# Performance work log

Measured on AMD Instinct MI355X. Metric: run time of the kernel, lower is better.

## Reference

```python
import jax, jax.numpy as jnp
import numpy as np

D_MODEL = 512
D_STATE = 128
D_CONV = 4
EXPAND = 2
NL = 10
HEADDIM = 64
D_INNER = EXPAND * D_MODEL            # 1024
NHEADS = D_INNER // HEADDIM           # 16
CONV_DIM = D_INNER + 2 * D_STATE      # 1280
D_PROJ = 2 * D_INNER + 2 * D_STATE + NHEADS  # 2320
BATCH = 8
IN_S, TOK_S = 3647, 64                # -> 57 tokens
IN_G, TOK_G = 18, 2                   # -> 9 tokens
NCLS = 55
CA_HEADS = 8
EPS = 1e-5


def setup_inputs() -> dict:
    key = jax.random.key(0)
    ks = iter(jax.random.split(key, 80))
    nrm = lambda shape, s=0.02: jax.random.normal(next(ks), shape, jnp.float32) * s
    inp = {
        "x_spectra": jax.random.normal(next(ks), (BATCH, IN_S), jnp.float32),
        "x_gaia": jax.random.normal(next(ks), (BATCH, IN_G), jnp.float32),
        "tok_w_s": nrm((TOK_S, D_MODEL), 0.05), "tok_b_s": jnp.zeros((D_MODEL,)),
        "tok_w_g": nrm((TOK_G, D_MODEL), 0.05), "tok_b_g": jnp.zeros((D_MODEL,)),
    }
    for p in ("ms", "mg"):  # spectra / gaia Mamba2 stacks, params stacked over layers
        inp[p + "_Win"] = nrm((NL, D_MODEL, D_PROJ))
        inp[p + "_conv_w"] = nrm((NL, CONV_DIM, D_CONV), 0.1)
        inp[p + "_conv_b"] = jnp.zeros((NL, CONV_DIM))
        inp[p + "_dt_bias"] = nrm((NL, NHEADS), 0.5)
        inp[p + "_A_log"] = jnp.log(jnp.tile(jnp.arange(1, NHEADS + 1, dtype=jnp.float32), (NL, 1)))
        inp[p + "_D"] = jnp.ones((NL, NHEADS))
        inp[p + "_norm_w"] = jnp.ones((NL, D_INNER))
        inp[p + "_Wout"] = nrm((NL, D_INNER, D_MODEL))
    for p in ("ca_s", "ca_g"):  # cross-attention blocks
        inp[p + "_ln_w"] = jnp.ones((D_MODEL,)); inp[p + "_ln_b"] = jnp.zeros((D_MODEL,))
        inp[p + "_in_w"] = nrm((3 * D_MODEL, D_MODEL)); inp[p + "_in_b"] = jnp.zeros((3 * D_MODEL,))
        inp[p + "_out_w"] = nrm((D_MODEL, D_MODEL)); inp[p + "_out_b"] = jnp.zeros((D_MODEL,))
    inp["cls_ln_w"] = jnp.ones((2 * D_MODEL,)); inp["cls_ln_b"] = jnp.zeros((2 * D_MODEL,))
    inp["cls_w"] = nrm((NCLS, 2 * D_MODEL)); inp["cls_b"] = jnp.zeros((NCLS,))
    return inp


def _ln(x, w, b):
    m = x.mean(-1, keepdims=True)
    v = jnp.var(x, -1, keepdims=True)
    return (x - m) * jax.lax.rsqrt(v + EPS) * w + b


def _tokenize(x, in_dim, tok_dim, w, b):
    bsz = x.shape[0]
    ntok = -(-in_dim // tok_dim)
    x = jnp.pad(x, ((0, 0), (0, ntok * tok_dim - in_dim)))
    return x.reshape(bsz, ntok, tok_dim) @ w + b  # [B, ntok, d_model]


def _mamba2_layer(x, Win, conv_w, conv_b, dt_bias, A_log, Dp, norm_w, Wout):
    bsz, L, _ = x.shape
    zxbcdt = x @ Win  # [B,L,D_PROJ]
    z, xBC, dt = jnp.split(zxbcdt, [D_INNER, D_INNER + CONV_DIM], axis=-1)
    # causal depthwise conv over time (kernel D_CONV), then SiLU
    xp = jnp.pad(xBC, ((0, 0), (D_CONV - 1, 0), (0, 0)))
    xBC = sum(conv_w[:, k] * xp[:, k:k + L, :] for k in range(D_CONV)) + conv_b
    xBC = jax.nn.silu(xBC)
    xh, Bm, Cm = jnp.split(xBC, [D_INNER, D_INNER + D_STATE], axis=-1)
    dt = jax.nn.softplus(dt + dt_bias)                 # [B,L,H]
    A = -jnp.exp(A_log)                                # [H]
    xh = xh.reshape(bsz, L, NHEADS, HEADDIM)
    dA = jnp.exp(dt * A)                               # [B,L,H] in (0,1)
    dBx = jnp.einsum('blh,bln,blhp->blhpn', dt, Bm, xh)
    # h_t = dA_t * h_{t-1} + dBx_t  via parallel associative scan over time
    def comb(e1, e2):
        a1, b1 = e1
        a2, b2 = e2
        return a1 * a2, a2[..., None, None] * b1 + b2
    _, h = jax.lax.associative_scan(comb, (dA, dBx), axis=1)  # h: [B,L,H,P,N]
    y = jnp.einsum('blhpn,bln->blhp', h, Cm) + Dp[None, None, :, None] * xh
    y = y.reshape(bsz, L, D_INNER)
    # gated RMSNorm (norm_before_gate=False): rmsnorm(y * silu(z)) * w
    y = y * jax.nn.silu(z)
    y = y * jax.lax.rsqrt(jnp.mean(y * y, -1, keepdims=True) + EPS) * norm_w
    return y @ Wout


def _mamba_stack(x, Win, cw, cb, dtb, Alog, Dp, nw, Wout):
    for i in range(NL):
        x = _mamba2_layer(x, Win[i], cw[i], cb[i], dtb[i], Alog[i], Dp[i], nw[i], Wout[i])
    return x


def _mha(q, kv, in_w, in_b, out_w, out_b):
    E = D_MODEL
    hd = E // CA_HEADS
    wq, wk, wv = in_w[:E], in_w[E:2 * E], in_w[2 * E:]
    bq, bk, bv = in_b[:E], in_b[E:2 * E], in_b[2 * E:]
    qh = (q @ wq.T + bq).reshape(*q.shape[:2], CA_HEADS, hd)
    kh = (kv @ wk.T + bk).reshape(*kv.shape[:2], CA_HEADS, hd)
    vh = (kv @ wv.T + bv).reshape(*kv.shape[:2], CA_HEADS, hd)
    scores = jnp.einsum('bqhd,bkhd->bhqk', qh, kh) / np.sqrt(hd).astype(np.float32)
    attn = jax.nn.softmax(scores, axis=-1)
    out = jnp.einsum('bhqk,bkhd->bqhd', attn, vh).reshape(*q.shape[:2], E)
    return out @ out_w.T + out_b


def reference(x_spectra, x_gaia, tok_w_s, tok_b_s, tok_w_g, tok_b_g,
              ms_Win, ms_conv_w, ms_conv_b, ms_dt_bias, ms_A_log, ms_D, ms_norm_w, ms_Wout,
              mg_Win, mg_conv_w, mg_conv_b, mg_dt_bias, mg_A_log, mg_D, mg_norm_w, mg_Wout,
              ca_s_ln_w, ca_s_ln_b, ca_s_in_w, ca_s_in_b, ca_s_out_w, ca_s_out_b,
              ca_g_ln_w, ca_g_ln_b, ca_g_in_w, ca_g_in_b, ca_g_out_w, ca_g_out_b,
              cls_ln_w, cls_ln_b, cls_w, cls_b):
    xs = _tokenize(x_spectra, IN_S, TOK_S, tok_w_s, tok_b_s)   # [B,57,512]
    xg = _tokenize(x_gaia, IN_G, TOK_G, tok_w_g, tok_b_g)      # [B,9,512]
    xs = _mamba_stack(xs, ms_Win, ms_conv_w, ms_conv_b, ms_dt_bias, ms_A_log, ms_D, ms_norm_w, ms_Wout)
    xg = _mamba_stack(xg, mg_Win, mg_conv_w, mg_conv_b, mg_dt_bias, mg_A_log, mg_D, mg_norm_w, mg_Wout)
    # cross attention (note: gaia attends to the UPDATED spectra, as in the torch code)
    xs = xs + _mha(_ln(xs, ca_s_ln_w, ca_s_ln_b), xg, ca_s_in_w, ca_s_in_b, ca_s_out_w, ca_s_out_b)
    xg = xg + _mha(_ln(xg, ca_g_ln_w, ca_g_ln_b), xs, ca_g_in_w, ca_g_in_b, ca_g_out_w, ca_g_out_b)
    fused = jnp.concatenate([xs.mean(1), xg.mean(1)], axis=-1)  # [B,1024]
    return _ln(fused, cls_ln_w, cls_ln_b) @ cls_w.T + cls_b      # [B,55]
```

## Files before the change

kernel.cpp:

```cpp
#include <hip/hip_runtime.h>
#include <cmath>

constexpr int BB    = 8;
constexpr int LS    = 57;
constexpr int LG    = 9;
constexpr int RS    = BB*LS;
constexpr int RG    = BB*LG;
constexpr int DM    = 512;
constexpr int DPROJ = 2320;
constexpr int DIN   = 1024;
constexpr int NH    = 16;
constexpr int HD    = 64;
constexpr int NLAY  = 10;

constexpr int SP_IN  = 4;
constexpr int SP_OUT = 8;
constexpr int SP_ATT = 4;

__device__ __forceinline__ float siluf(float x){ return x / (1.f + expf(-x)); }

typedef short  short8 __attribute__((ext_vector_type(8)));
typedef float  f32x4  __attribute__((ext_vector_type(4)));

__device__ __forceinline__ unsigned short f2bh(float f){
    unsigned int u = __float_as_uint(f);
    u = u + 0x7FFFu + ((u >> 16) & 1u);
    return (unsigned short)(u >> 16);
}
__device__ __forceinline__ float bh2f(unsigned short h){
    return __uint_as_float(((unsigned int)h) << 16);
}

__global__ __launch_bounds__(512) void tokenize_k(
    const float* __restrict__ x, const float* __restrict__ w, const float* __restrict__ bias,
    float* __restrict__ out, int in_dim, int tok_dim, int ntok)
{
    int t = blockIdx.x, b = blockIdx.y, d = threadIdx.x;
    __shared__ float xv[64];
    if (d < tok_dim) {
        int idx = t*tok_dim + d;
        xv[d] = (idx < in_dim) ? x[(size_t)b*in_dim + idx] : 0.f;
    }
    __syncthreads();
    float acc = bias[d];
    for (int k=0;k<tok_dim;k++) acc += xv[k]*w[(size_t)k*DM + d];
    out[(size_t)(b*ntok + t)*DM + d] = acc;
}

struct GemmJob {
    const float* A; const float* B; float* part; int M;
};

template<bool TB, int NSPLIT>
__global__ __launch_bounds__(256) void gemm_mfma(GemmJob j0, GemmJob j1, GemmJob j2, int N, int K)
{
    const int z = blockIdx.z;
    const int job = z / NSPLIT, split = z % NSPLIT;
    GemmJob jb = (job==0) ? j0 : (job==1 ? j1 : j2);
    const int bm = blockIdx.y*64, bn = blockIdx.x*64;
    const int M = jb.M;
    if (bm >= M) return;

    constexpr int SR = 40;
    __shared__ unsigned short Ah[64*SR], Al[64*SR];
    __shared__ unsigned short Bh[64*SR], Bl[64*SR];

    const int tid = threadIdx.x;
    const float* __restrict__ A  = jb.A;
    const float* __restrict__ Bm = jb.B;

    const int ar = tid >> 2, ac0 = (tid & 3) * 8;
    const int wkN = tid >> 3, wcN0 = (tid & 7) * 8;
    const int wnT = tid >> 2, wkT0 = (tid & 3) * 8;

    float a_reg[8];
    float w_reg[8];

    auto loadA = [&](int k0){
        if (bm + ar < M){
            const float* src = A + (size_t)(bm+ar)*K + k0 + ac0;
            float4 v0 = *(const float4*)(src);
            float4 v1 = *(const float4*)(src+4);
            a_reg[0]=v0.x; a_reg[1]=v0.y; a_reg[2]=v0.z; a_reg[3]=v0.w;
            a_reg[4]=v1.x; a_reg[5]=v1.y; a_reg[6]=v1.z; a_reg[7]=v1.w;
        } else {
            #pragma unroll
            for (int j=0;j<8;j++) a_reg[j]=0.f;
        }
    };
    auto loadW = [&](int k0){
        if constexpr (!TB){
            const float* src = Bm + (size_t)(k0+wkN)*N + bn + wcN0;
            if (bn + wcN0 + 4 <= N){
                float4 v0 = *(const float4*)(src);
                float4 v1 = *(const float4*)(src+4);
                w_reg[0]=v0.x; w_reg[1]=v0.y; w_reg[2]=v0.z; w_reg[3]=v0.w;
                w_reg[4]=v1.x; w_reg[5]=v1.y; w_reg[6]=v1.z; w_reg[7]=v1.w;
            } else if (bn + wcN0 < N){
                float4 v0 = *(const float4*)(src);
                w_reg[0]=v0.x; w_reg[1]=v0.y; w_reg[2]=v0.z; w_reg[3]=v0.w;
                w_reg[4]=0.f; w_reg[5]=0.f; w_reg[6]=0.f; w_reg[7]=0.f;
            } else {
                #pragma unroll
                for (int j=0;j<8;j++) w_reg[j]=0.f;
            }
        } else {
            if (bn + wnT < N){
                const float* src = Bm + (size_t)(bn+wnT)*K + k0 + wkT0;
                float4 v0 = *(const float4*)(src);
                float4 v1 = *(const float4*)(src+4);
                w_reg[0]=v0.x; w_reg[1]=v0.y; w_reg[2]=v0.z; w_reg[3]=v0.w;
                w_reg[4]=v1.x; w_reg[5]=v1.y; w_reg[6]=v1.z; w_reg[7]=v1.w;
            } else {
                #pragma unroll
                for (int j=0;j<8;j++) w_reg[j]=0.f;
            }
        }
    };
    auto storeT = [&](){
        #pragma unroll
        for (int j=0;j<8;j++){
            const unsigned short h = f2bh(a_reg[j]);
            const unsigned short lo = f2bh(a_reg[j] - bh2f(h));
            Ah[ar*SR + ac0 + j] = h;
            Al[ar*SR + ac0 + j] = lo;
        }
        if constexpr (!TB){
            #pragma unroll
            for (int j=0;j<8;j++){
                const unsigned short h = f2bh(w_reg[j]);
                const unsigned short lo = f2bh(w_reg[j] - bh2f(h));
                Bh[(wcN0+j)*SR + wkN] = h;
                Bl[(wcN0+j)*SR + wkN] = lo;
            }
        } else {
            #pragma unroll
            for (int j=0;j<8;j++){
                const unsigned short h = f2bh(w_reg[j]);
                const unsigned short lo = f2bh(w_reg[j] - bh2f(h));
                Bh[wnT*SR + wkT0 + j] = h;
                Bl[wnT*SR + wkT0 + j] = lo;
            }
        }
    };

    const int Kper = K / NSPLIT;
    const int koff = split * Kper;
    const int nk   = Kper / 32;

    const int l  = tid & 63, w = tid >> 6;
    const int fr = l & 15, kg = (l >> 4) * 8;

    f32x4 acc0 = {0.f,0.f,0.f,0.f};
    f32x4 acc1 = {0.f,0.f,0.f,0.f};
    f32x4 acc2 = {0.f,0.f,0.f,0.f};
    f32x4 acc3 = {0.f,0.f,0.f,0.f};

    loadA(koff); loadW(koff);
    for (int t=0; t<nk; ++t){
        storeT();
        __syncthreads();
        if (t+1 < nk){ loadA(koff+(t+1)*32); loadW(koff+(t+1)*32); }

        const short8 ah = *(const short8*)&Ah[(w*16+fr)*SR + kg];
        const short8 al = *(const short8*)&Al[(w*16+fr)*SR + kg];
        {
            const short8 bh = *(const short8*)&Bh[(fr)*SR + kg];
            const short8 bl = *(const short8*)&Bl[(fr)*SR + kg];
            acc0 = __builtin_amdgcn_mfma_f32_16x16x32_bf16(ah, bh, acc0, 0,0,0);
            acc0 = __builtin_amdgcn_mfma_f32_16x16x32_bf16(ah, bl, acc0, 0,0,0);
            acc0 = __builtin_amdgcn_mfma_f32_16x16x32_bf16(al, bh, acc0, 0,0,0);
        }
        {
            const short8 bh = *(const short8*)&Bh[(16+fr)*SR + kg];
            const short8 bl = *(const short8*)&Bl[(16+fr)*SR + kg];
            acc1 = __builtin_amdgcn_mfma_f32_16x16x32_bf16(ah, bh, acc1, 0,0,0);
            acc1 = __builtin_amdgcn_mfma_f32_16x16x32_bf16(ah, bl, acc1, 0,0,0);
            acc1 = __builtin_amdgcn_mfma_f32_16x16x32_bf16(al, bh, acc1, 0,0,0);
        }
        {
            const short8 bh = *(const short8*)&Bh[(32+fr)*SR + kg];
            const short8 bl = *(const short8*)&Bl[(32+fr)*SR + kg];
            acc2 = __builtin_amdgcn_mfma_f32_16x16x32_bf16(ah, bh, acc2, 0,0,0);
            acc2 = __builtin_amdgcn_mfma_f32_16x16x32_bf16(ah, bl, acc2, 0,0,0);
            acc2 = __builtin_amdgcn_mfma_f32_16x16x32_bf16(al, bh, acc2, 0,0,0);
        }
        {
            const short8 bh = *(const short8*)&Bh[(48+fr)*SR + kg];
            const short8 bl = *(const short8*)&Bl[(48+fr)*SR + kg];
            acc3 = __builtin_amdgcn_mfma_f32_16x16x32_bf16(ah, bh, acc3, 0,0,0);
            acc3 = __builtin_amdgcn_mfma_f32_16x16x32_bf16(ah, bl, acc3, 0,0,0);
            acc3 = __builtin_amdgcn_mfma_f32_16x16x32_bf16(al, bh, acc3, 0,0,0);
        }
        __syncthreads();
    }

    float* __restrict__ P = jb.part + (size_t)split*M*N;
    const int rbase = bm + w*16 + (l>>4)*4;
    #pragma unroll
    for (int nt=0; nt<4; ++nt){
        const f32x4 a = (nt==0)?acc0 : (nt==1)?acc1 : (nt==2)?acc2 : acc3;
        const int n = bn + nt*16 + fr;
        if (n < N){
            #pragma unroll
            for (int j=0;j<4;j++){
                const int m = rbase + j;
                if (m < M) P[(size_t)m*N + n] = a[j];
            }
        }
    }
}

struct RJob { const float* part; const float* bias; const float* res; float* C; int M; };

template<int NS>
__global__ __launch_bounds__(256) void reduce_k(RJob j0, RJob j1, int N)
{
    RJob j = blockIdx.y ? j1 : j0;
    const size_t total = (size_t)j.M*N;
    const size_t i4 = ((size_t)blockIdx.x*256 + threadIdx.x)*4;
    if (i4 >= total) return;
    float4 s = *(const float4*)(j.part + i4);
    #pragma unroll
    for (int t=1;t<NS;t++){
        const float4 v = *(const float4*)(j.part + (size_t)t*total + i4);
        s.x+=v.x; s.y+=v.y; s.z+=v.z; s.w+=v.w;
    }
    const int n = (int)(i4 % (size_t)N);
    if (j.bias){ s.x+=j.bias[n]; s.y+=j.bias[n+1]; s.z+=j.bias[n+2]; s.w+=j.bias[n+3]; }
    if (j.res){ const float4 r = *(const float4*)(j.res + i4); s.x+=r.x; s.y+=r.y; s.z+=r.z; s.w+=r.w; }
    *(float4*)(j.C + i4) = s;
}

template<int NS>
__global__ __launch_bounds__(256) void reduce_k3(RJob j0, RJob j1, RJob j2, int N)
{
    RJob j = (blockIdx.y==0) ? j0 : (blockIdx.y==1 ? j1 : j2);
    const size_t total = (size_t)j.M*N;
    const size_t i4 = ((size_t)blockIdx.x*256 + threadIdx.x)*4;
    if (i4 >= total) return;
    float4 s = *(const float4*)(j.part + i4);
    #pragma unroll
    for (int t=1;t<NS;t++){
        const float4 v = *(const float4*)(j.part + (size_t)t*total + i4);
        s.x+=v.x; s.y+=v.y; s.z+=v.z; s.w+=v.w;
    }
    const int n = (int)(i4 % (size_t)N);
    if (j.bias){ s.x+=j.bias[n]; s.y+=j.bias[n+1]; s.z+=j.bias[n+2]; s.w+=j.bias[n+3]; }
    if (j.res){ const float4 r = *(const float4*)(j.res + i4); s.x+=r.x; s.y+=r.y; s.z+=r.z; s.w+=r.w; }
    *(float4*)(j.C + i4) = s;
}

struct PrepJob {
    const float* part;
    float* zsilu; float* xh; float* Bc; float* Cc; float* dtw;
    const float* cw; const float* cb; const float* dtb;
    int R, L;
};

__device__ __forceinline__ float4 psum4(const float* p, size_t pstr){
    float4 a = *(const float4*)p;
    const float4 b = *(const float4*)(p + pstr);
    const float4 c = *(const float4*)(p + 2*pstr);
    const float4 d = *(const float4*)(p + 3*pstr);
    a.x += b.x + c.x + d.x;
    a.y += b.y + c.y + d.y;
    a.z += b.z + c.z + d.z;
    a.w += b.w + c.w + d.w;
    return a;
}

__global__ __launch_bounds__(256) void mamba_prep(PrepJob js, PrepJob jg)
{
    PrepJob j = blockIdx.y ? jg : js;
    const int R = j.R, L = j.L;
    constexpr int QPR = 580;
    const int q = blockIdx.x*256 + threadIdx.x;
    if (q >= R*QPR) return;
    const int r = q / QPR, qi = q % QPR;
    const int l = r % L;
    const size_t pstr = (size_t)R*DPROJ;
    const float* base = j.part + (size_t)r*DPROJ;

    if (qi < 256) {
        const int c = qi*4;
        float4 s = psum4(base + c, pstr);
        s.x = siluf(s.x); s.y = siluf(s.y); s.z = siluf(s.z); s.w = siluf(s.w);
        *(float4*)(j.zsilu + (size_t)r*1024 + c) = s;
    } else if (qi < 576) {
        const int cc = (qi-256)*4;
        float tk[4][4];
        #pragma unroll
        for (int k=0;k<4;k++){
            const int lr = l - 3 + k;
            if (lr >= 0){
                float4 v = psum4(j.part + (size_t)(r-3+k)*DPROJ + 1024 + cc, pstr);
                tk[k][0]=v.x; tk[k][1]=v.y; tk[k][2]=v.z; tk[k][3]=v.w;
            } else {
                tk[k][0]=0.f; tk[k][1]=0.f; tk[k][2]=0.f; tk[k][3]=0.f;
            }
        }
        const float4 cb4 = *(const float4*)(j.cb + cc);
        const float cba[4] = {cb4.x, cb4.y, cb4.z, cb4.w};
        float out[4];
        #pragma unroll
        for (int jj=0;jj<4;jj++){
            const float4 wv = *(const float4*)(j.cw + (size_t)(cc+jj)*4);
            float v = cba[jj] + wv.x*tk[0][jj] + wv.y*tk[1][jj]
                              + wv.z*tk[2][jj] + wv.w*tk[3][jj];
            out[jj] = siluf(v);
        }
        float4 o4; o4.x=out[0]; o4.y=out[1]; o4.z=out[2]; o4.w=out[3];
        if (cc < 1024)       *(float4*)(j.xh + (size_t)r*1024 + cc)        = o4;
        else if (cc < 1152)  *(float4*)(j.Bc + (size_t)r*128 + (cc-1024))  = o4;
        else                 *(float4*)(j.Cc + (size_t)r*128 + (cc-1152))  = o4;
    } else {
        const int hd = (qi-576)*4;
        float4 s = psum4(base + 2304 + hd, pstr);
        const float4 b4 = *(const float4*)(j.dtb + hd);
        float raw[4] = {s.x+b4.x, s.y+b4.y, s.z+b4.z, s.w+b4.w};
        float4 o4;
        float* op = &o4.x;
        #pragma unroll
        for (int jj=0;jj<4;jj++)
            op[jj] = (raw[jj] > 20.f) ? raw[jj] : log1pf(expf(raw[jj]));
        *(float4*)(j.dtw + (size_t)r*16 + hd) = o4;
    }
}

__global__ __launch_bounds__(256) void mamba_cbt(
    const float* __restrict__ Bc_s, const float* __restrict__ Cc_s, float* __restrict__ cbt_s,
    const float* __restrict__ Bc_g, const float* __restrict__ Cc_g, float* __restrict__ cbt_g)
{
    const int b = blockIdx.x, st = blockIdx.y;
    const float* Bc = st ? Bc_g : Bc_s;
    const float* Cc = st ? Cc_g : Cc_s;
    float* cbt = st ? cbt_g : cbt_s;
    const int L = st ? LG : LS;
    constexpr int SB = 132;
    __shared__ float Bm[64*SB], Cm[64*SB];
    const int t = threadIdx.x;
    for (int idx = t; idx < L*32; idx += 256){
        const int l = idx >> 5, c4 = (idx & 31)*4;
        *(float4*)&Bm[l*SB + c4] = *(const float4*)(Bc + (size_t)(b*L+l)*128 + c4);
        *(float4*)&Cm[l*SB + c4] = *(const float4*)(Cc + (size_t)(b*L+l)*128 + c4);
    }
    __syncthreads();
    const int ti = t >> 4, tj = t & 15;
    float acc[4][4] = {};
    for (int k0=0;k0<128;k0+=4){
        float4 cr[4], br[4];
        #pragma unroll
        for (int a=0;a<4;a++) cr[a] = *(const float4*)&Cm[(ti+16*a)*SB + k0];
        #pragma unroll
        for (int qq=0;qq<4;qq++) br[qq] = *(const float4*)&Bm[(tj+16*qq)*SB + k0];
        #pragma unroll
        for (int a=0;a<4;a++)
            #pragma unroll
            for (int qq=0;qq<4;qq++)
                acc[a][qq] += cr[a].x*br[qq].x + cr[a].y*br[qq].y
                            + cr[a].z*br[qq].z + cr[a].w*br[qq].w;
    }
    #pragma unroll
    for (int a=0;a<4;a++){
        const int i = ti + 16*a;
        if (i < L){
            #pragma unroll
            for (int qq=0;qq<4;qq++){
                const int jj = tj + 16*qq;
                if (jj < L) cbt[(size_t)b*3840 + i*60 + jj] = acc[a][qq];
            }
        }
    }
}

__global__ __launch_bounds__(256) void mamba_y(
    const float* __restrict__ cbt_s, const float* __restrict__ xh_s, const float* __restrict__ dtw_s,
    const float* __restrict__ al_s, const float* __restrict__ Dw_s, float* __restrict__ y_s,
    const float* __restrict__ cbt_g, const float* __restrict__ xh_g, const float* __restrict__ dtw_g,
    const float* __restrict__ al_g, const float* __restrict__ Dw_g, float* __restrict__ y_g)
{
    const int h = blockIdx.x, b = blockIdx.y, st = blockIdx.z;
    const float* cbt = st ? cbt_g : cbt_s;
    const float* xh  = st ? xh_g  : xh_s;
    const float* dtw = st ? dtw_g : dtw_s;
    const float* al  = st ? al_g  : al_s;
    const float* Dw  = st ? Dw_g  : Dw_s;
    float* y = st ? y_g : y_s;
    const int L = st ? LG : LS;

    const int t = threadIdx.x;
    constexpr int SG = 60, SX = 68;
    __shared__ float Gm[64*SG], Xm[64*SX];
    __shared__ float dts[64], sps[64];

    const float Ah = -expf(al[h]);
    const float Dh = Dw[h];

    if (t < 64){
        float dtv = (t < L) ? dtw[(size_t)(b*L+t)*16 + h] : 0.f;
        float s = dtv;
        #pragma unroll
        for (int d=1; d<64; d<<=1){
            float o = __shfl_up(s, d, 64);
            if (t >= d) s += o;
        }
        dts[t] = dtv; sps[t] = s;
    }
    for (int idx = t; idx < L*16; idx += 256){
        const int l = idx >> 4, c4 = (idx & 15)*4;
        *(float4*)&Xm[l*SX + c4] = *(const float4*)(xh + (size_t)(b*L+l)*1024 + h*64 + c4);
    }
    __syncthreads();

    for (int idx = t; idx < L*15; idx += 256){
        const int i = idx/15, j4 = (idx%15)*4;
        const float4 v = *(const float4*)(cbt + (size_t)b*3840 + i*60 + j4);
        const float va[4] = {v.x, v.y, v.z, v.w};
        float g[4];
        const float si = sps[i];
        #pragma unroll
        for (int jj=0;jj<4;jj++){
            const int jc = j4 + jj;
            float gg = 0.f;
            if (jc <= i && jc < L)
                gg = expf(Ah*(si - sps[jc])) * dts[jc] * va[jj];
            g[jj] = gg;
        }
        float4 g4; g4.x=g[0]; g4.y=g[1]; g4.z=g[2]; g4.w=g[3];
        *(float4*)&Gm[i*SG + j4] = g4;
    }
    __syncthreads();

    const int ti = t >> 4, tj = t & 15;
    int la[4];
    #pragma unroll
    for (int a=0;a<4;a++) la[a] = ti + 16*a;
    float accY[4][4] = {};
    for (int m=0; m<L; ++m){
        float xr[4], gr[4];
        #pragma unroll
        for (int qq=0;qq<4;qq++) xr[qq] = Xm[m*SX + tj + 16*qq];
        #pragma unroll
        for (int a=0;a<4;a++) gr[a] = (la[a] < L) ? Gm[la[a]*SG + m] : 0.f;
        #pragma unroll
        for (int a=0;a<4;a++)
            #pragma unroll
            for (int qq=0;qq<4;qq++) accY[a][qq] = fmaf(gr[a], xr[qq], accY[a][qq]);
    }
    #pragma unroll
    for (int a=0;a<4;a++){
        if (la[a] < L){
            float* yrow = y + (size_t)(b*L + la[a])*DIN + h*HD;
            #pragma unroll
            for (int qq=0;qq<4;qq++){
                const int col = tj + 16*qq;
                yrow[col] = accY[a][qq] + Dh * Xm[la[a]*SX + col];
            }
        }
    }
}

__global__ __launch_bounds__(256) void gated_rmsnorm(
    const float* __restrict__ y_s, const float* __restrict__ zs_s, const float* __restrict__ nw_s, float* __restrict__ o_s,
    const float* __restrict__ y_g, const float* __restrict__ zs_g, const float* __restrict__ nw_g, float* __restrict__ o_g)
{
    int r = blockIdx.x, t = threadIdx.x;
    int st = (r >= RS);
    int row = st ? r - RS : r;
    const float* y  = (st ? y_g  : y_s) + (size_t)row*DIN;
    const float* zs = (st ? zs_g : zs_s) + (size_t)row*DIN;
    const float* nw = st ? nw_g : nw_s;
    float* o = (st ? o_g : o_s) + (size_t)row*DIN;

    float g[4]; float s2 = 0.f;
    #pragma unroll
    for (int i=0;i<4;i++){
        int idx = t + i*256;
        float gv = y[idx] * zs[idx];
        g[i] = gv; s2 += gv*gv;
    }
    #pragma unroll
    for (int o2=32;o2;o2>>=1) s2 += __shfl_xor(s2, o2, 64);
    __shared__ float red[4];
    if ((t & 63) == 0) red[t>>6] = s2;
    __syncthreads();
    float S2 = red[0]+red[1]+red[2]+red[3];
    float scale = rsqrtf(S2*(1.f/DIN) + 1e-5f);
    #pragma unroll
    for (int i=0;i<4;i++){
        int idx = t + i*256;
        o[idx] = g[i]*scale*nw[idx];
    }
}

__global__ __launch_bounds__(256) void ln_rows(
    const float* __restrict__ x, const float* __restrict__ w, const float* __restrict__ b,
    float* __restrict__ out, int D)
{
    int r = blockIdx.x, t = threadIdx.x;
    const float* xr = x + (size_t)r*D;
    float s = 0.f, s2 = 0.f;
    for (int i=t;i<D;i+=256){ float v = xr[i]; s += v; s2 += v*v; }
    #pragma unroll
    for (int o=32;o;o>>=1){ s += __shfl_xor(s,o,64); s2 += __shfl_xor(s2,o,64); }
    __shared__ float red[8];
    if ((t & 63) == 0){ red[t>>6] = s; red[4+(t>>6)] = s2; }
    __syncthreads();
    float S  = red[0]+red[1]+red[2]+red[3];
    float S2 = red[4]+red[5]+red[6]+red[7];
    float mean = S/D;
    float var  = S2/D - mean*mean;
    float inv  = rsqrtf(var + 1e-5f);
    for (int i=t;i<D;i+=256)
        out[(size_t)r*D + i] = (xr[i]-mean)*inv*w[i] + b[i];
}

template<int LQ, int LKV>
__global__ __launch_bounds__(256) void mha_attn2(
    const float* __restrict__ qh, const float* __restrict__ kh,
    const float* __restrict__ vh, float* __restrict__ out)
{
    const int hh = blockIdx.x, b = blockIdx.y, t = threadIdx.x;
    constexpr int SD = 68;
    constexpr int SS = 60;
    constexpr int QT = (LQ +15)/16;
    constexpr int KT = (LKV+15)/16;
    __shared__ float Qs[LQ*SD];
    __shared__ float Ks[LKV*SD];
    __shared__ float Vs[LKV*SD];
    __shared__ float Ps[LQ*SS];

    for (int idx = t; idx < LQ*16; idx += 256){
        const int r = idx>>4, c4 = (idx&15)*4;
        *(float4*)&Qs[r*SD+c4] = *(const float4*)(qh + (size_t)(b*LQ+r)*DM + hh*64 + c4);
    }
    for (int idx = t; idx < LKV*16; idx += 256){
        const int r = idx>>4, c4 = (idx&15)*4;
        *(float4*)&Ks[r*SD+c4] = *(const float4*)(kh + (size_t)(b*LKV+r)*DM + hh*64 + c4);
        *(float4*)&Vs[r*SD+c4] = *(const float4*)(vh + (size_t)(b*LKV+r)*DM + hh*64 + c4);
    }
    __syncthreads();

    const int ti = t>>4, tj = t&15;

    {
        float acc[QT][KT];
        #pragma unroll
        for (int a=0;a<QT;a++)
            #pragma unroll
            for (int q=0;q<KT;q++) acc[a][q] = 0.f;
        for (int k0=0;k0<64;k0+=4){
            float4 qr[QT], kr[KT];
            #pragma unroll
            for (int a=0;a<QT;a++){
                int rr = ti+16*a; if (rr >= LQ) rr = LQ-1;
                qr[a] = *(const float4*)&Qs[rr*SD+k0];
            }
            #pragma unroll
            for (int q=0;q<KT;q++){
                int rr = tj+16*q; if (rr >= LKV) rr = LKV-1;
                kr[q] = *(const float4*)&Ks[rr*SD+k0];
            }
            #pragma unroll
            for (int a=0;a<QT;a++)
                #pragma unroll
                for (int q=0;q<KT;q++)
                    acc[a][q] += qr[a].x*kr[q].x + qr[a].y*kr[q].y
                               + qr[a].z*kr[q].z + qr[a].w*kr[q].w;
        }
        #pragma unroll
        for (int a=0;a<QT;a++){
            const int i = ti+16*a;
            if (i < LQ){
                #pragma unroll
                for (int q=0;q<KT;q++){
                    const int jj = tj+16*q;
                    if (jj < LKV) Ps[i*SS+jj] = acc[a][q]*0.125f;
                }
            }
        }
    }
    __syncthreads();

    if (t < LQ){
        float mx = -1e30f;
        for (int j=0;j<LKV;j++) mx = fmaxf(mx, Ps[t*SS+j]);
        float se = 0.f;
        for (int j=0;j<LKV;j++){ float e = expf(Ps[t*SS+j]-mx); Ps[t*SS+j] = e; se += e; }
        const float inv = 1.f/se;
        for (int j=0;j<LKV;j++) Ps[t*SS+j] *= inv;
    }
    __syncthreads();

    {
        float o[QT][4];
        #pragma unroll
        for (int a=0;a<QT;a++){ o[a][0]=0.f; o[a][1]=0.f; o[a][2]=0.f; o[a][3]=0.f; }
        for (int m=0;m<LKV;m++){
            const float4 vv = *(const float4*)&Vs[m*SD + tj*4];
            #pragma unroll
            for (int a=0;a<QT;a++){
                const int rr = ti+16*a;
                const float pv = (rr < LQ) ? Ps[rr*SS+m] : 0.f;
                o[a][0] = fmaf(pv, vv.x, o[a][0]);
                o[a][1] = fmaf(pv, vv.y, o[a][1]);
                o[a][2] = fmaf(pv, vv.z, o[a][2]);
                o[a][3] = fmaf(pv, vv.w, o[a][3]);
            }
        }
        #pragma unroll
        for (int a=0;a<QT;a++){
            const int rr = ti+16*a;
            if (rr < LQ){
                float4 o4; o4.x=o[a][0]; o4.y=o[a][1]; o4.z=o[a][2]; o4.w=o[a][3];
                *(float4*)(out + (size_t)(b*LQ+rr)*DM + hh*64 + tj*4) = o4;
            }
        }
    }
}

__global__ __launch_bounds__(512) void head_fused(
    const float* __restrict__ xs, const float* __restrict__ xg,
    const float* __restrict__ lw, const float* __restrict__ lb,
    const float* __restrict__ cw, const float* __restrict__ cb,
    float* __restrict__ out)
{
    const int b = blockIdx.x, t = threadIdx.x;
    __shared__ float fr[1024];
    __shared__ float red[16];
    __shared__ float pr[55*8];
    {
        float s = 0.f;
        for (int l=0;l<LS;l++) s += xs[(size_t)(b*LS+l)*DM + t];
        fr[t] = s*(1.f/LS);
        float g = 0.f;
        for (int l=0;l<LG;l++) g += xg[(size_t)(b*LG+l)*DM + t];
        fr[512+t] = g*(1.f/LG);
    }
    __syncthreads();
    float v0 = fr[t], v1 = fr[512+t];
    float sm = v0+v1, sq = v0*v0 + v1*v1;
    #pragma unroll
    for (int o=32;o;o>>=1){ sm += __shfl_xor(sm,o,64); sq += __shfl_xor(sq,o,64); }
    if ((t&63)==0){ red[t>>6] = sm; red[8+(t>>6)] = sq; }
    __syncthreads();
    float S=0.f, Q=0.f;
    #pragma unroll
    for (int i=0;i<8;i++){ S += red[i]; Q += red[8+i]; }
    const float mean = S*(1.f/1024.f);
    const float var  = Q*(1.f/1024.f) - mean*mean;
    const float inv  = rsqrtf(var + 1e-5f);
    fr[t]     = (v0-mean)*inv*lw[t]     + lb[t];
    fr[512+t] = (v1-mean)*inv*lw[512+t] + lb[512+t];
    __syncthreads();
    {
        const int c = t & 63, pp = t >> 6;
        if (c < 55){
            float a = 0.f;
            const float* wr = cw + (size_t)c*1024 + pp*128;
            const float* xr = fr + pp*128;
            #pragma unroll 4
            for (int k=0;k<128;k++) a = fmaf(xr[k], wr[k], a);
            pr[c*8+pp] = a;
        }
    }
    __syncthreads();
    if (t < 55){
        float a = cb[t];
        #pragma unroll
        for (int p2=0;p2<8;p2++) a += pr[t*8+p2];
        out[b*55 + t] = a;
    }
}

extern "C" void kernel_launch(void* const* d_in, const int* in_sizes, int n_in,
                              void* d_out, int out_size, void* d_ws, size_t ws_size,
                              hipStream_t stream)
{
    (void)in_sizes; (void)n_in; (void)out_size; (void)ws_size;
    const float* x_spectra = (const float*)d_in[0];
    const float* x_gaia    = (const float*)d_in[1];
    const float* tok_w_s   = (const float*)d_in[2];
    const float* tok_b_s   = (const float*)d_in[3];
    const float* tok_w_g   = (const float*)d_in[4];
    const float* tok_b_g   = (const float*)d_in[5];
    const float* ms_Win    = (const float*)d_in[6];
    const float* ms_conv_w = (const float*)d_in[7];
    const float* ms_conv_b = (const float*)d_in[8];
    const float* ms_dtb    = (const float*)d_in[9];
    const float* ms_Alog   = (const float*)d_in[10];
    const float* ms_D      = (const float*)d_in[11];
    const float* ms_nw     = (const float*)d_in[12];
    const float* ms_Wout   = (const float*)d_in[13];
    const float* mg_Win    = (const float*)d_in[14];
    const float* mg_conv_w = (const float*)d_in[15];
    const float* mg_conv_b = (const float*)d_in[16];
    const float* mg_dtb    = (const float*)d_in[17];
    const float* mg_Alog   = (const float*)d_in[18];
    const float* mg_D      = (const float*)d_in[19];
    const float* mg_nw     = (const float*)d_in[20];
    const float* mg_Wout   = (const float*)d_in[21];
    const float* cas_ln_w  = (const float*)d_in[22];
    const float* cas_ln_b  = (const float*)d_in[23];
    const float* cas_in_w  = (const float*)d_in[24];
    const float* cas_in_b  = (const float*)d_in[25];
    const float* cas_out_w = (const float*)d_in[26];
    const float* cas_out_b = (const float*)d_in[27];
    const float* cag_ln_w  = (const float*)d_in[28];
    const float* cag_ln_b  = (const float*)d_in[29];
    const float* cag_in_w  = (const float*)d_in[30];
    const float* cag_in_b  = (const float*)d_in[31];
    const float* cag_out_w = (const float*)d_in[32];
    const float* cag_out_b = (const float*)d_in[33];
    const float* cls_ln_w  = (const float*)d_in[34];
    const float* cls_ln_b  = (const float*)d_in[35];
    const float* cls_w     = (const float*)d_in[36];
    const float* cls_b     = (const float*)d_in[37];

    float* p = (float*)d_ws;
    auto alloc = [&](size_t n){ float* r = p; p += n; return r; };
    float* xs       = alloc((size_t)RS*DM);
    float* xg       = alloc((size_t)RG*DM);
    float* y_s      = alloc((size_t)RS*DIN);
    float* y_g      = alloc((size_t)RG*DIN);
    float* yn_s     = alloc((size_t)RS*DIN);
    float* yn_g     = alloc((size_t)RG*DIN);
    float* lnbuf    = alloc((size_t)RS*DM);
    float* attn_out = alloc((size_t)RS*DM);
    float* part_inS  = alloc((size_t)SP_IN*RS*DPROJ);
    float* part_inG  = alloc((size_t)SP_IN*RG*DPROJ);
    float* part_outS = alloc((size_t)SP_OUT*RS*DM);
    float* part_outG = alloc((size_t)SP_OUT*RG*DM);
    float* uni       = alloc((size_t)3*SP_ATT*RS*DM);
    float* zsilu_s = uni;
    float* zsilu_g = zsilu_s + (size_t)RS*1024;
    float* xh_s    = zsilu_g + (size_t)RG*1024;
    float* xh_g    = xh_s    + (size_t)RS*1024;
    float* Bc_s    = xh_g    + (size_t)RG*1024;
    float* Bc_g    = Bc_s    + (size_t)RS*128;
    float* Cc_s    = Bc_g    + (size_t)RG*128;
    float* Cc_g    = Cc_s    + (size_t)RS*128;
    float* dtw_s   = Cc_g    + (size_t)RG*128;
    float* dtw_g   = dtw_s   + (size_t)RS*16;
    float* cbt_s   = dtw_g   + (size_t)RG*16;
    float* cbt_g   = cbt_s   + (size_t)BB*3840;
    float* part_q = uni;
    float* part_k = uni + (size_t)SP_ATT*RS*DM;
    float* part_v = uni + (size_t)2*SP_ATT*RS*DM;
    float* qh = y_s;
    float* vh = y_s + (size_t)RS*DM;
    float* kh = yn_s;

    tokenize_k<<<dim3(LS,BB), 512, 0, stream>>>(x_spectra, tok_w_s, tok_b_s, xs, 3647, 64, LS);
    tokenize_k<<<dim3(LG,BB), 512, 0, stream>>>(x_gaia,    tok_w_g, tok_b_g, xg, 18,   2,  LG);

    const int rblkS = (RS*DM + 1023)/1024;
    const int prepBlk = (RS*580 + 255)/256;
    const int NTI = (DPROJ + 63)/64;

    for (int i=0;i<NLAY;i++){
        const float* Win_s  = ms_Win  + (size_t)i*DM*DPROJ;
        const float* Win_g  = mg_Win  + (size_t)i*DM*DPROJ;
        const float* cw_s   = ms_conv_w + (size_t)i*1280*4;
        const float* cw_g   = mg_conv_w + (size_t)i*1280*4;
        const float* cbv_s  = ms_conv_b + (size_t)i*1280;
        const float* cbv_g  = mg_conv_b + (size_t)i*1280;
        const float* dtb_s  = ms_dtb  + (size_t)i*NH;
        const float* dtb_g  = mg_dtb  + (size_t)i*NH;
        const float* al_s   = ms_Alog + (size_t)i*NH;
        const float* al_g   = mg_Alog + (size_t)i*NH;
        const float* Dw_s   = ms_D    + (size_t)i*NH;
        const float* Dw_g   = mg_D    + (size_t)i*NH;
        const float* nw_s   = ms_nw   + (size_t)i*DIN;
        const float* nw_g   = mg_nw   + (size_t)i*DIN;
        const float* Wout_s = ms_Wout + (size_t)i*DIN*DM;
        const float* Wout_g = mg_Wout + (size_t)i*DIN*DM;

        GemmJob inS{xs, Win_s, part_inS, RS};
        GemmJob inG{xg, Win_g, part_inG, RG};
        gemm_mfma<false,SP_IN><<<dim3(NTI, 8, 2*SP_IN), 256, 0, stream>>>(
            inS, inG, inG, DPROJ, DM);

        PrepJob pjS{part_inS, zsilu_s, xh_s, Bc_s, Cc_s, dtw_s, cw_s, cbv_s, dtb_s, RS, LS};
        PrepJob pjG{part_inG, zsilu_g, xh_g, Bc_g, Cc_g, dtw_g, cw_g, cbv_g, dtb_g, RG, LG};
        mamba_prep<<<dim3(prepBlk, 2), 256, 0, stream>>>(pjS, pjG);

        mamba_cbt<<<dim3(BB, 2), 256, 0, stream>>>(Bc_s, Cc_s, cbt_s, Bc_g, Cc_g, cbt_g);

        mamba_y<<<dim3(NH, BB, 2), 256, 0, stream>>>(
            cbt_s, xh_s, dtw_s, al_s, Dw_s, y_s,
            cbt_g, xh_g, dtw_g, al_g, Dw_g, y_g);

        gated_rmsnorm<<<dim3(RS+RG), 256, 0, stream>>>(
            y_s, zsilu_s, nw_s, yn_s,  y_g, zsilu_g, nw_g, yn_g);

        GemmJob outS{yn_s, Wout_s, part_outS, RS};
        GemmJob outG{yn_g, Wout_g, part_outG, RG};
        gemm_mfma<false,SP_OUT><<<dim3(DM/64, 8, 2*SP_OUT), 256, 0, stream>>>(
            outS, outG, outG, DM, DIN);

        RJob roS{part_outS, nullptr, nullptr, xs, RS};
        RJob roG{part_outG, nullptr, nullptr, xg, RG};
        reduce_k<SP_OUT><<<dim3(rblkS, 2), 256, 0, stream>>>(roS, roG, DM);
    }

    {
        ln_rows<<<dim3(RS), 256, 0, stream>>>(xs, cas_ln_w, cas_ln_b, lnbuf, DM);
        GemmJob jq{lnbuf, cas_in_w,            part_q, RS};
        GemmJob jk{xg,    cas_in_w +  512*512, part_k, RG};
        GemmJob jv{xg,    cas_in_w + 1024*512, part_v, RG};
        gemm_mfma<true,SP_ATT><<<dim3(DM/64, 8, 3*SP_ATT), 256, 0, stream>>>(jq, jk, jv, DM, DM);
        RJob rq{part_q, cas_in_b,      nullptr, qh, RS};
        RJob rk{part_k, cas_in_b+512,  nullptr, kh, RG};
        RJob rv{part_v, cas_in_b+1024, nullptr, vh, RG};
        reduce_k3<SP_ATT><<<dim3(rblkS, 3), 256, 0, stream>>>(rq, rk, rv, DM);
        mha_attn2<LS,LG><<<dim3(8,BB), 256, 0, stream>>>(qh, kh, vh, attn_out);
        GemmJob jo{attn_out, cas_out_w, part_outS, RS};
        gemm_mfma<true,SP_ATT><<<dim3(DM/64, 8, SP_ATT), 256, 0, stream>>>(jo, jo, jo, DM, DM);
        RJob ro{part_outS, cas_out_b, xs, xs, RS};
        reduce_k<SP_ATT><<<dim3(rblkS, 1), 256, 0, stream>>>(ro, ro, DM);
    }

    {
        ln_rows<<<dim3(RG), 256, 0, stream>>>(xg, cag_ln_w, cag_ln_b, lnbuf, DM);
        GemmJob jq{lnbuf, cag_in_w,            part_q, RG};
        GemmJob jk{xs,    cag_in_w +  512*512, part_k, RS};
        GemmJob jv{xs,    cag_in_w + 1024*512, part_v, RS};
        gemm_mfma<true,SP_ATT><<<dim3(DM/64, 8, 3*SP_ATT), 256, 0, stream>>>(jq, jk, jv, DM, DM);
        RJob rq{part_q, cag_in_b,      nullptr, qh, RG};
        RJob rk{part_k, cag_in_b+512,  nullptr, kh, RS};
        RJob rv{part_v, cag_in_b+1024, nullptr, vh, RS};
        reduce_k3<SP_ATT><<<dim3(rblkS, 3), 256, 0, stream>>>(rq, rk, rv, DM);
        mha_attn2<LG,LS><<<dim3(8,BB), 256, 0, stream>>>(qh, kh, vh, attn_out);
        GemmJob jo{attn_out, cag_out_w, part_outS, RG};
        gemm_mfma<true,SP_ATT><<<dim3(DM/64, 2, SP_ATT), 256, 0, stream>>>(jo, jo, jo, DM, DM);
        RJob ro{part_outS, cag_out_b, xg, xg, RG};
        reduce_k<SP_ATT><<<dim3((RG*DM+1023)/1024, 1), 256, 0, stream>>>(ro, ro, DM);
    }

    head_fused<<<dim3(BB), 512, 0, stream>>>(xs, xg, cls_ln_w, cls_ln_b, cls_w, cls_b, (float*)d_out);
}
```

Baseline: 839.0 us.

## Pre-split weights and activations into bf16 hi/lo and double-buffer GEMM LDS

A conversion pass at the start of each call turns all Mamba in/out projection and cross-attention weights into bf16 hi/lo pairs, stored K-contiguous (transposed). Producer kernels (tokenize, reduce, gated RMSNorm, layernorm, attention) now emit activations directly as hi/lo bf16. The GEMM therefore only copies short8 vectors into a double-buffered LDS tile, with one barrier per k-step, instead of converting and scattering fp32 values inside the main loop. The input-projection split-K drops from 4 to 2, so the prep step sums two partials. In exchange, every call now pays an extra full pass over about 34M weight values, and the GEMM still reads the same number of weight bytes as before.

```diff
diff --git a/kernel.cpp b/kernel.cpp
--- a/kernel.cpp
+++ b/kernel.cpp
@@ -13,14 +13,15 @@
 constexpr int HD    = 64;
 constexpr int NLAY  = 10;
 
-constexpr int SP_IN  = 4;
+constexpr int SP_IN  = 2;
 constexpr int SP_OUT = 8;
 constexpr int SP_ATT = 4;
 
 __device__ __forceinline__ float siluf(float x){ return x / (1.f + expf(-x)); }
 
-typedef short  short8 __attribute__((ext_vector_type(8)));
-typedef float  f32x4  __attribute__((ext_vector_type(4)));
+typedef short  short8  __attribute__((ext_vector_type(8)));
+typedef short  short4_ __attribute__((ext_vector_type(4)));
+typedef float  f32x4   __attribute__((ext_vector_type(4)));
 
 __device__ __forceinline__ unsigned short f2bh(float f){
     unsigned int u = __float_as_uint(f);
@@ -33,7 +34,8 @@
 
 __global__ __launch_bounds__(512) void tokenize_k(
     const float* __restrict__ x, const float* __restrict__ w, const float* __restrict__ bias,
-    float* __restrict__ out, int in_dim, int tok_dim, int ntok)
+    float* __restrict__ out, unsigned short* __restrict__ outh, unsigned short* __restrict__ outl,
+    int in_dim, int tok_dim, int ntok)
 {
     int t = blockIdx.x, b = blockIdx.y, d = threadIdx.x;
     __shared__ float xv[64];
@@ -44,14 +46,100 @@
     __syncthreads();
     float acc = bias[d];
     for (int k=0;k<tok_dim;k++) acc += xv[k]*w[(size_t)k*DM + d];
-    out[(size_t)(b*ntok + t)*DM + d] = acc;
+    const size_t o = (size_t)(b*ntok + t)*DM + d;
+    out[o] = acc;
+    const unsigned short h = f2bh(acc);
+    outh[o] = h;
+    outl[o] = f2bh(acc - bh2f(h));
+}
+
+__global__ __launch_bounds__(256) void convert_all_w(
+    const float* __restrict__ winS, const float* __restrict__ winG,
+    const float* __restrict__ woutS, const float* __restrict__ woutG,
+    unsigned short* __restrict__ winh, unsigned short* __restrict__ winl,
+    unsigned short* __restrict__ wouth, unsigned short* __restrict__ woutl)
+{
+    const int z = blockIdx.z;
+    const float* src; unsigned short *dh, *dl; int K, N;
+    if (z < 20){
+        const int layer = z >> 1, s = z & 1;
+        src = (s ? winG : winS) + (size_t)layer*DM*DPROJ;
+        K = DM; N = DPROJ;
+        dh = winh + (size_t)z*DPROJ*DM;
+        dl = winl + (size_t)z*DPROJ*DM;
+    } else {
+        const int i = z - 20, layer = i >> 1, s = i & 1;
+        src = (s ? woutG : woutS) + (size_t)layer*DIN*DM;
+        K = DIN; N = DM;
+        dh = wouth + (size_t)i*DM*DIN;
+        dl = woutl + (size_t)i*DM*DIN;
+    }
+    const int nt = blockIdx.x*64, kt = blockIdx.y*64;
+    if (nt >= N || kt >= K) return;
+    __shared__ float tile[64][65];
+    const int tid = threadIdx.x;
+    #pragma unroll
+    for (int i=0;i<4;i++){
+        const int kk = (tid>>4) + i*16;
+        const int c4 = (tid&15)*4;
+        const int n = nt + c4;
+        float4 v = {0.f,0.f,0.f,0.f};
+        if (n + 3 < N) v = *(const float4*)(src + (size_t)(kt+kk)*N + n);
+        else {
+            if (n   < N) v.x = src[(size_t)(kt+kk)*N + n];
+            if (n+1 < N) v.y = src[(size_t)(kt+kk)*N + n+1];
+            if (n+2 < N) v.z = src[(size_t)(kt+kk)*N + n+2];
+            if (n+3 < N) v.w = src[(size_t)(kt+kk)*N + n+3];
+        }
+        tile[kk][c4]=v.x; tile[kk][c4+1]=v.y; tile[kk][c4+2]=v.z; tile[kk][c4+3]=v.w;
+    }
+    __syncthreads();
+    #pragma unroll
+    for (int i=0;i<2;i++){
+        const int c = tid + i*256;
+        const int n = c >> 3, k8 = (c & 7)*8;
+        if (nt + n < N){
+            short8 vh_, vl_;
+            #pragma unroll
+            for (int q=0;q<8;q++){
+                const float f = tile[k8+q][n];
+                const unsigned short h = f2bh(f);
+                vh_[q] = (short)h;
+                vl_[q] = (short)f2bh(f - bh2f(h));
+            }
+            *(short8*)(dh + (size_t)(nt+n)*K + kt + k8) = vh_;
+            *(short8*)(dl + (size_t)(nt+n)*K + kt + k8) = vl_;
+        }
+    }
+}
+
+struct CvtE { const float* src; unsigned short* h; unsigned short* l; int n; };
+
+__global__ __launch_bounds__(256) void convert_wE(CvtE j0, CvtE j1, CvtE j2, CvtE j3)
+{
+    CvtE j = (blockIdx.y==0)?j0 : (blockIdx.y==1)?j1 : (blockIdx.y==2)?j2 : j3;
+    const int i4 = (blockIdx.x*256 + threadIdx.x)*4;
+    if (i4 >= j.n) return;
+    const float4 v = *(const float4*)(j.src + i4);
+    const float f[4] = {v.x,v.y,v.z,v.w};
+    short4_ h4, l4;
+    #pragma unroll
+    for (int q=0;q<4;q++){
+        const unsigned short h = f2bh(f[q]);
+        h4[q] = (short)h;
+        l4[q] = (short)f2bh(f[q] - bh2f(h));
+    }
+    *(short4_*)(j.h + i4) = h4;
+    *(short4_*)(j.l + i4) = l4;
 }
 
 struct GemmJob {
-    const float* A; const float* B; float* part; int M;
+    const unsigned short* Ah; const unsigned short* Al;
+    const unsigned short* Wh; const unsigned short* Wl;
+    float* part; int M;
 };
 
-template<bool TB, int NSPLIT>
+template<int NSPLIT>
 __global__ __launch_bounds__(256) void gemm_mfma(GemmJob j0, GemmJob j1, GemmJob j2, int N, int K)
 {
     const int z = blockIdx.z;
@@ -62,136 +150,88 @@
     if (bm >= M) return;
 
     constexpr int SR = 40;
-    __shared__ unsigned short Ah[64*SR], Al[64*SR];
-    __shared__ unsigned short Bh[64*SR], Bl[64*SR];
+    __shared__ unsigned short AhS[2][64*SR], AlS[2][64*SR];
+    __shared__ unsigned short BhS[2][64*SR], BlS[2][64*SR];
 
     const int tid = threadIdx.x;
-    const float* __restrict__ A  = jb.A;
-    const float* __restrict__ Bm = jb.B;
-
-    const int ar = tid >> 2, ac0 = (tid & 3) * 8;
-    const int wkN = tid >> 3, wcN0 = (tid & 7) * 8;
-    const int wnT = tid >> 2, wkT0 = (tid & 3) * 8;
-
-    float a_reg[8];
-    float w_reg[8];
-
-    auto loadA = [&](int k0){
-        if (bm + ar < M){
-            const float* src = A + (size_t)(bm+ar)*K + k0 + ac0;
-            float4 v0 = *(const float4*)(src);
-            float4 v1 = *(const float4*)(src+4);
-            a_reg[0]=v0.x; a_reg[1]=v0.y; a_reg[2]=v0.z; a_reg[3]=v0.w;
-            a_reg[4]=v1.x; a_reg[5]=v1.y; a_reg[6]=v1.z; a_reg[7]=v1.w;
-        } else {
-            #pragma unroll
-            for (int j=0;j<8;j++) a_reg[j]=0.f;
-        }
+    const int r0 = tid >> 2, k0off = (tid & 3)*8;
+    const bool aok = (bm + r0 < M);
+    const bool wok = (bn + r0 < N);
+    const unsigned short* Aph = jb.Ah + (size_t)(bm+r0)*K;
+    const unsigned short* Apl = jb.Al + (size_t)(bm+r0)*K;
+    const unsigned short* Wph = jb.Wh + (size_t)(bn+r0)*K;
+    const unsigned short* Wpl = jb.Wl + (size_t)(bn+r0)*K;
+
+    const short8 z8 = {0,0,0,0,0,0,0,0};
+    short8 ra_h = z8, ra_l = z8, rw_h = z8, rw_l = z8;
+
+    auto loadT = [&](int k0){
+        if (aok){
+            ra_h = *(const short8*)(Aph + k0 + k0off);
+            ra_l = *(const short8*)(Apl + k0 + k0off);
+        } else { ra_h = z8; ra_l = z8; }
+        if (wok){
+            rw_h = *(const short8*)(Wph + k0 + k0off);
+            rw_l = *(const short8*)(Wpl + k0 + k0off);
+        } else { rw_h = z8; rw_l = z8; }
     };
-    auto loadW = [&](int k0){
-        if constexpr (!TB){
-            const float* src = Bm + (size_t)(k0+wkN)*N + bn + wcN0;
-            if (bn + wcN0 + 4 <= N){
-                float4 v0 = *(const float4*)(src);
-                float4 v1 = *(const float4*)(src+4);
-                w_reg[0]=v0.x; w_reg[1]=v0.y; w_reg[2]=v0.z; w_reg[3]=v0.w;
-                w_reg[4]=v1.x; w_reg[5]=v1.y; w_reg[6]=v1.z; w_reg[7]=v1.w;
-            } else if (bn + wcN0 < N){
-                float4 v0 = *(const float4*)(src);
-                w_reg[0]=v0.x; w_reg[1]=v0.y; w_reg[2]=v0.z; w_reg[3]=v0.w;
-                w_reg[4]=0.f; w_reg[5]=0.f; w_reg[6]=0.f; w_reg[7]=0.f;
-            } else {
-                #pragma unroll
-                for (int j=0;j<8;j++) w_reg[j]=0.f;
-            }
-        } else {
-            if (bn + wnT < N){
-                const float* src = Bm + (size_t)(bn+wnT)*K + k0 + wkT0;
-                float4 v0 = *(const float4*)(src);
-                float4 v1 = *(const float4*)(src+4);
-                w_reg[0]=v0.x; w_reg[1]=v0.y; w_reg[2]=v0.z; w_reg[3]=v0.w;
-                w_reg[4]=v1.x; w_reg[5]=v1.y; w_reg[6]=v1.z; w_reg[7]=v1.w;
-            } else {
-                #pragma unroll
-                for (int j=0;j<8;j++) w_reg[j]=0.f;
-            }
-        }
-    };
-    auto storeT = [&](){
-        #pragma unroll
-        for (int j=0;j<8;j++){
-            const unsigned short h = f2bh(a_reg[j]);
-            const unsigned short lo = f2bh(a_reg[j] - bh2f(h));
-            Ah[ar*SR + ac0 + j] = h;
-            Al[ar*SR + ac0 + j] = lo;
-        }
-        if constexpr (!TB){
-            #pragma unroll
-            for (int j=0;j<8;j++){
-                const unsigned short h = f2bh(w_reg[j]);
-                const unsigned short lo = f2bh(w_reg[j] - bh2f(h));
-                Bh[(wcN0+j)*SR + wkN] = h;
-                Bl[(wcN0+j)*SR + wkN] = lo;
-            }
-        } else {
-            #pragma unroll
-            for (int j=0;j<8;j++){
-                const unsigned short h = f2bh(w_reg[j]);
-                const unsigned short lo = f2bh(w_reg[j] - bh2f(h));
-                Bh[wnT*SR + wkT0 + j] = h;
-                Bl[wnT*SR + wkT0 + j] = lo;
-            }
-        }
+    auto storeT = [&](int buf){
+        *(short8*)&AhS[buf][r0*SR + k0off] = ra_h;
+        *(short8*)&AlS[buf][r0*SR + k0off] = ra_l;
+        *(short8*)&BhS[buf][r0*SR + k0off] = rw_h;
+        *(short8*)&BlS[buf][r0*SR + k0off] = rw_l;
     };
 
     const int Kper = K / NSPLIT;
     const int koff = split * Kper;
-    const int nk   = Kper / 32;
-
-    const int l  = tid & 63, w = tid >> 6;
-    const int fr = l & 15, kg = (l >> 4) * 8;
+    const int nk = Kper / 32;
+
+    const int l = tid & 63, w = tid >> 6;
+    const int fr = l & 15, kg = (l >> 4)*8;
 
     f32x4 acc0 = {0.f,0.f,0.f,0.f};
     f32x4 acc1 = {0.f,0.f,0.f,0.f};
     f32x4 acc2 = {0.f,0.f,0.f,0.f};
     f32x4 acc3 = {0.f,0.f,0.f,0.f};
 
-    loadA(koff); loadW(koff);
+    loadT(koff);
+    storeT(0);
+    __syncthreads();
     for (int t=0; t<nk; ++t){
-        storeT();
-        __syncthreads();
-        if (t+1 < nk){ loadA(koff+(t+1)*32); loadW(koff+(t+1)*32); }
-
-        const short8 ah = *(const short8*)&Ah[(w*16+fr)*SR + kg];
-        const short8 al = *(const short8*)&Al[(w*16+fr)*SR + kg];
+        const int cur = t & 1;
+        if (t+1 < nk) loadT(koff + (t+1)*32);
+
+        const short8 ah = *(const short8*)&AhS[cur][(w*16+fr)*SR + kg];
+        const short8 al = *(const short8*)&AlS[cur][(w*16+fr)*SR + kg];
         {
-            const short8 bh = *(const short8*)&Bh[(fr)*SR + kg];
-            const short8 bl = *(const short8*)&Bl[(fr)*SR + kg];
+            const short8 bh = *(const short8*)&BhS[cur][(fr)*SR + kg];
+            const short8 bl = *(const short8*)&BlS[cur][(fr)*SR + kg];
             acc0 = __builtin_amdgcn_mfma_f32_16x16x32_bf16(ah, bh, acc0, 0,0,0);
             acc0 = __builtin_amdgcn_mfma_f32_16x16x32_bf16(ah, bl, acc0, 0,0,0);
             acc0 = __builtin_amdgcn_mfma_f32_16x16x32_bf16(al, bh, acc0, 0,0,0);
         }
         {
-            const short8 bh = *(const short8*)&Bh[(16+fr)*SR + kg];
-            const short8 bl = *(const short8*)&Bl[(16+fr)*SR + kg];
+            const short8 bh = *(const short8*)&BhS[cur][(16+fr)*SR + kg];
+            const short8 bl = *(const short8*)&BlS[cur][(16+fr)*SR + kg];
             acc1 = __builtin_amdgcn_mfma_f32_16x16x32_bf16(ah, bh, acc1, 0,0,0);
             acc1 = __builtin_amdgcn_mfma_f32_16x16x32_bf16(ah, bl, acc1, 0,0,0);
             acc1 = __builtin_amdgcn_mfma_f32_16x16x32_bf16(al, bh, acc1, 0,0,0);
         }
         {
-            const short8 bh = *(const short8*)&Bh[(32+fr)*SR + kg];
-            const short8 bl = *(const short8*)&Bl[(32+fr)*SR + kg];
+            const short8 bh = *(const short8*)&BhS[cur][(32+fr)*SR + kg];
+            const short8 bl = *(const short8*)&BlS[cur][(32+fr)*SR + kg];
             acc2 = __builtin_amdgcn_mfma_f32_16x16x32_bf16(ah, bh, acc2, 0,0,0);
             acc2 = __builtin_amdgcn_mfma_f32_16x16x32_bf16(ah, bl, acc2, 0,0,0);
             acc2 = __builtin_amdgcn_mfma_f32_16x16x32_bf16(al, bh, acc2, 0,0,0);
         }
         {
-            const short8 bh = *(const short8*)&Bh[(48+fr)*SR + kg];
-            const short8 bl = *(const short8*)&Bl[(48+fr)*SR + kg];
+            const short8 bh = *(const short8*)&BhS[cur][(48+fr)*SR + kg];
+            const short8 bl = *(const short8*)&BlS[cur][(48+fr)*SR + kg];
             acc3 = __builtin_amdgcn_mfma_f32_16x16x32_bf16(ah, bh, acc3, 0,0,0);
             acc3 = __builtin_amdgcn_mfma_f32_16x16x32_bf16(ah, bl, acc3, 0,0,0);
             acc3 = __builtin_amdgcn_mfma_f32_16x16x32_bf16(al, bh, acc3, 0,0,0);
         }
+        if (t+1 < nk) storeT(cur^1);
         __syncthreads();
     }
 
@@ -211,7 +251,8 @@
     }
 }
 
-struct RJob { const float* part; const float* bias; const float* res; float* C; int M; };
+struct RJob { const float* part; const float* bias; const float* res; float* C;
+              unsigned short* ph; unsigned short* pl; int M; };
 
 template<int NS>
 __global__ __launch_bounds__(256) void reduce_k(RJob j0, RJob j1, int N)
@@ -229,7 +270,19 @@
     const int n = (int)(i4 % (size_t)N);
     if (j.bias){ s.x+=j.bias[n]; s.y+=j.bias[n+1]; s.z+=j.bias[n+2]; s.w+=j.bias[n+3]; }
     if (j.res){ const float4 r = *(const float4*)(j.res + i4); s.x+=r.x; s.y+=r.y; s.z+=r.z; s.w+=r.w; }
-    *(float4*)(j.C + i4) = s;
+    if (j.C) *(float4*)(j.C + i4) = s;
+    if (j.ph){
+        const float f[4] = {s.x, s.y, s.z, s.w};
+        short4_ h4, l4;
+        #pragma unroll
+        for (int q=0;q<4;q++){
+            const unsigned short h = f2bh(f[q]);
+            h4[q] = (short)h;
+            l4[q] = (short)f2bh(f[q] - bh2f(h));
+        }
+        *(short4_*)(j.ph + i4) = h4;
+        *(short4_*)(j.pl + i4) = l4;
+    }
 }
 
 template<int NS>
@@ -258,15 +311,10 @@
     int R, L;
 };
 
-__device__ __forceinline__ float4 psum4(const float* p, size_t pstr){
+__device__ __forceinline__ float4 psum2(const float* p, size_t pstr){
     float4 a = *(const float4*)p;
     const float4 b = *(const float4*)(p + pstr);
-    const float4 c = *(const float4*)(p + 2*pstr);
-    const float4 d = *(const float4*)(p + 3*pstr);
-    a.x += b.x + c.x + d.x;
-    a.y += b.y + c.y + d.y;
-    a.z += b.z + c.z + d.z;
-    a.w += b.w + c.w + d.w;
+    a.x += b.x; a.y += b.y; a.z += b.z; a.w += b.w;
     return a;
 }
 
@@ -284,7 +332,7 @@
 
     if (qi < 256) {
         const int c = qi*4;
-        float4 s = psum4(base + c, pstr);
+        float4 s = psum2(base + c, pstr);
         s.x = siluf(s.x); s.y = siluf(s.y); s.z = siluf(s.z); s.w = siluf(s.w);
         *(float4*)(j.zsilu + (size_t)r*1024 + c) = s;
     } else if (qi < 576) {
@@ -294,7 +342,7 @@
         for (int k=0;k<4;k++){
             const int lr = l - 3 + k;
             if (lr >= 0){
-                float4 v = psum4(j.part + (size_t)(r-3+k)*DPROJ + 1024 + cc, pstr);
+                float4 v = psum2(j.part + (size_t)(r-3+k)*DPROJ + 1024 + cc, pstr);
                 tk[k][0]=v.x; tk[k][1]=v.y; tk[k][2]=v.z; tk[k][3]=v.w;
             } else {
                 tk[k][0]=0.f; tk[k][1]=0.f; tk[k][2]=0.f; tk[k][3]=0.f;
@@ -316,7 +364,7 @@
         else                 *(float4*)(j.Cc + (size_t)r*128 + (cc-1152))  = o4;
     } else {
         const int hd = (qi-576)*4;
-        float4 s = psum4(base + 2304 + hd, pstr);
+        float4 s = psum2(base + 2304 + hd, pstr);
         const float4 b4 = *(const float4*)(j.dtb + hd);
         float raw[4] = {s.x+b4.x, s.y+b4.y, s.z+b4.z, s.w+b4.w};
         float4 o4;
@@ -462,8 +510,10 @@
 }
 
 __global__ __launch_bounds__(256) void gated_rmsnorm(
-    const float* __restrict__ y_s, const float* __restrict__ zs_s, const float* __restrict__ nw_s, float* __restrict__ o_s,
-    const float* __restrict__ y_g, const float* __restrict__ zs_g, const float* __restrict__ nw_g, float* __restrict__ o_g)
+    const float* __restrict__ y_s, const float* __restrict__ zs_s, const float* __restrict__ nw_s,
+    unsigned short* __restrict__ oh_s, unsigned short* __restrict__ ol_s,
+    const float* __restrict__ y_g, const float* __restrict__ zs_g, const float* __restrict__ nw_g,
+    unsigned short* __restrict__ oh_g, unsigned short* __restrict__ ol_g)
 {
     int r = blockIdx.x, t = threadIdx.x;
     int st = (r >= RS);
@@ -471,7 +521,8 @@
     const float* y  = (st ? y_g  : y_s) + (size_t)row*DIN;
     const float* zs = (st ? zs_g : zs_s) + (size_t)row*DIN;
     const float* nw = st ? nw_g : nw_s;
-    float* o = (st ? o_g : o_s) + (size_t)row*DIN;
+    unsigned short* oh = (st ? oh_g : oh_s) + (size_t)row*DIN;
+    unsigned short* ol = (st ? ol_g : ol_s) + (size_t)row*DIN;
 
     float g[4]; float s2 = 0.f;
     #pragma unroll
@@ -490,13 +541,16 @@
     #pragma unroll
     for (int i=0;i<4;i++){
         int idx = t + i*256;
-        o[idx] = g[i]*scale*nw[idx];
+        const float val = g[i]*scale*nw[idx];
+        const unsigned short h = f2bh(val);
+        oh[idx] = h;
+        ol[idx] = f2bh(val - bh2f(h));
     }
 }
 
 __global__ __launch_bounds__(256) void ln_rows(
     const float* __restrict__ x, const float* __restrict__ w, const float* __restrict__ b,
-    float* __restrict__ out, int D)
+    unsigned short* __restrict__ outh, unsigned short* __restrict__ outl, int D)
 {
     int r = blockIdx.x, t = threadIdx.x;
     const float* xr = x + (size_t)r*D;
@@ -512,14 +566,19 @@
     float mean = S/D;
     float var  = S2/D - mean*mean;
     float inv  = rsqrtf(var + 1e-5f);
-    for (int i=t;i<D;i+=256)
-        out[(size_t)r*D + i] = (xr[i]-mean)*inv*w[i] + b[i];
+    for (int i=t;i<D;i+=256){
+        const float val = (xr[i]-mean)*inv*w[i] + b[i];
+        const unsigned short h = f2bh(val);
+        outh[(size_t)r*D + i] = h;
+        outl[(size_t)r*D + i] = f2bh(val - bh2f(h));
+    }
 }
 
 template<int LQ, int LKV>
 __global__ __launch_bounds__(256) void mha_attn2(
     const float* __restrict__ qh, const float* __restrict__ kh,
-    const float* __restrict__ vh, float* __restrict__ out)
+    const float* __restrict__ vh,
+    unsigned short* __restrict__ outh, unsigned short* __restrict__ outl)
 {
     const int hh = blockIdx.x, b = blockIdx.y, t = threadIdx.x;
     constexpr int SD = 68;
@@ -613,8 +672,16 @@
         for (int a=0;a<QT;a++){
             const int rr = ti+16*a;
             if (rr < LQ){
-                float4 o4; o4.x=o[a][0]; o4.y=o[a][1]; o4.z=o[a][2]; o4.w=o[a][3];
-                *(float4*)(out + (size_t)(b*LQ+rr)*DM + hh*64 + tj*4) = o4;
+                short4_ h4, l4;
+                #pragma unroll
+                for (int q=0;q<4;q++){
+                    const unsigned short h = f2bh(o[a][q]);
+                    h4[q] = (short)h;
+                    l4[q] = (short)f2bh(o[a][q] - bh2f(h));
+                }
+                const size_t off = (size_t)(b*LQ+rr)*DM + hh*64 + tj*4;
+                *(short4_*)(outh + off) = h4;
+                *(short4_*)(outl + off) = l4;
             }
         }
     }
@@ -724,44 +791,71 @@
     float* xg       = alloc((size_t)RG*DM);
     float* y_s      = alloc((size_t)RS*DIN);
     float* y_g      = alloc((size_t)RG*DIN);
-    float* yn_s     = alloc((size_t)RS*DIN);
-    float* yn_g     = alloc((size_t)RG*DIN);
-    float* lnbuf    = alloc((size_t)RS*DM);
-    float* attn_out = alloc((size_t)RS*DM);
+    float* qh       = alloc((size_t)RS*DM);
+    float* kh       = alloc((size_t)RS*DM);
+    float* vh       = alloc((size_t)RS*DM);
     float* part_inS  = alloc((size_t)SP_IN*RS*DPROJ);
     float* part_inG  = alloc((size_t)SP_IN*RG*DPROJ);
     float* part_outS = alloc((size_t)SP_OUT*RS*DM);
     float* part_outG = alloc((size_t)SP_OUT*RG*DM);
-    float* uni       = alloc((size_t)3*SP_ATT*RS*DM);
-    float* zsilu_s = uni;
-    float* zsilu_g = zsilu_s + (size_t)RS*1024;
-    float* xh_s    = zsilu_g + (size_t)RG*1024;
-    float* xh_g    = xh_s    + (size_t)RS*1024;
-    float* Bc_s    = xh_g    + (size_t)RG*1024;
-    float* Bc_g    = Bc_s    + (size_t)RS*128;
-    float* Cc_s    = Bc_g    + (size_t)RG*128;
-    float* Cc_g    = Cc_s    + (size_t)RS*128;
-    float* dtw_s   = Cc_g    + (size_t)RG*128;
-    float* dtw_g   = dtw_s   + (size_t)RS*16;
-    float* cbt_s   = dtw_g   + (size_t)RG*16;
-    float* cbt_g   = cbt_s   + (size_t)BB*3840;
-    float* part_q = uni;
-    float* part_k = uni + (size_t)SP_ATT*RS*DM;
-    float* part_v = uni + (size_t)2*SP_ATT*RS*DM;
-    float* qh = y_s;
-    float* vh = y_s + (size_t)RS*DM;
-    float* kh = yn_s;
-
-    tokenize_k<<<dim3(LS,BB), 512, 0, stream>>>(x_spectra, tok_w_s, tok_b_s, xs, 3647, 64, LS);
-    tokenize_k<<<dim3(LG,BB), 512, 0, stream>>>(x_gaia,    tok_w_g, tok_b_g, xg, 18,   2,  LG);
+    float* part_q    = alloc((size_t)SP_ATT*RS*DM);
+    float* part_k    = alloc((size_t)SP_ATT*RS*DM);
+    float* part_v    = alloc((size_t)SP_ATT*RS*DM);
+    float* zsilu_s = alloc((size_t)RS*1024);
+    float* zsilu_g = alloc((size_t)RG*1024);
+    float* xh_s    = alloc((size_t)RS*1024);
+    float* xh_g    = alloc((size_t)RG*1024);
+    float* Bc_s    = alloc((size_t)RS*128);
+    float* Bc_g    = alloc((size_t)RG*128);
+    float* Cc_s    = alloc((size_t)RS*128);
+    float* Cc_g    = alloc((size_t)RG*128);
+    float* dtw_s   = alloc((size_t)RS*16);
+    float* dtw_g   = alloc((size_t)RG*16);
+    float* cbt_s   = alloc((size_t)BB*3840);
+    float* cbt_g   = alloc((size_t)BB*3840);
+
+    unsigned short* up = (unsigned short*)p;
+    auto ualloc = [&](size_t n){ unsigned short* r = up; up += n; return r; };
+    unsigned short* xsh   = ualloc((size_t)RS*DM);
+    unsigned short* xsl   = ualloc((size_t)RS*DM);
+    unsigned short* xgh   = ualloc((size_t)RG*DM);
+    unsigned short* xgl   = ualloc((size_t)RG*DM);
+    unsigned short* ynh_s = ualloc((size_t)RS*DIN);
+    unsigned short* ynl_s = ualloc((size_t)RS*DIN);
+    unsigned short* ynh_g = ualloc((size_t)RG*DIN);
+    unsigned short* ynl_g = ualloc((size_t)RG*DIN);
+    unsigned short* lnh   = ualloc((size_t)RS*DM);
+    unsigned short* lnl   = ualloc((size_t)RS*DM);
+    unsigned short* aoh   = ualloc((size_t)RS*DM);
+    unsigned short* aol   = ualloc((size_t)RS*DM);
+    unsigned short* caih  = ualloc((size_t)1536*512);
+    unsigned short* cail  = ualloc((size_t)1536*512);
+    unsigned short* caoh  = ualloc((size_t)512*512);
+    unsigned short* caol  = ualloc((size_t)512*512);
+    unsigned short* cgih  = ualloc((size_t)1536*512);
+    unsigned short* cgil  = ualloc((size_t)1536*512);
+    unsigned short* cgoh  = ualloc((size_t)512*512);
+    unsigned short* cgol  = ualloc((size_t)512*512);
+    unsigned short* winh  = ualloc((size_t)20*DPROJ*DM);
+    unsigned short* winl  = ualloc((size_t)20*DPROJ*DM);
+    unsigned short* wouth = ualloc((size_t)20*DM*DIN);
+    unsigned short* woutl = ualloc((size_t)20*DM*DIN);
+
+    CvtE e0{cas_in_w,  caih, cail, 1536*512};
+    CvtE e1{cas_out_w, caoh, caol, 512*512};
+    CvtE e2{cag_in_w,  cgih, cgil, 1536*512};
+    CvtE e3{cag_out_w, cgoh, cgol, 512*512};
+    convert_wE<<<dim3(768, 4), 256, 0, stream>>>(e0, e1, e2, e3);
+    convert_all_w<<<dim3(37, 16, 40), 256, 0, stream>>>(
+        ms_Win, mg_Win, ms_Wout, mg_Wout, winh, winl, wouth, woutl);
+
+    tokenize_k<<<dim3(LS,BB), 512, 0, stream>>>(x_spectra, tok_w_s, tok_b_s, xs, xsh, xsl, 3647, 64, LS);
+    tokenize_k<<<dim3(LG,BB), 512, 0, stream>>>(x_gaia,    tok_w_g, tok_b_g, xg, xgh, xgl, 18,   2,  LG);
 
     const int rblkS = (RS*DM + 1023)/1024;
     const int prepBlk = (RS*580 + 255)/256;
-    const int NTI = (DPROJ + 63)/64;
 
     for (int i=0;i<NLAY;i++){
-        const float* Win_s  = ms_Win  + (size_t)i*DM*DPROJ;
-        const float* Win_g  = mg_Win  + (size_t)i*DM*DPROJ;
         const float* cw_s   = ms_conv_w + (size_t)i*1280*4;
         const float* cw_g   = mg_conv_w + (size_t)i*1280*4;
         const float* cbv_s  = ms_conv_b + (size_t)i*1280;
@@ -774,13 +868,19 @@
         const float* Dw_g   = mg_D    + (size_t)i*NH;
         const float* nw_s   = ms_nw   + (size_t)i*DIN;
         const float* nw_g   = mg_nw   + (size_t)i*DIN;
-        const float* Wout_s = ms_Wout + (size_t)i*DIN*DM;
-        const float* Wout_g = mg_Wout + (size_t)i*DIN*DM;
-
-        GemmJob inS{xs, Win_s, part_inS, RS};
-        GemmJob inG{xg, Win_g, part_inG, RG};
-        gemm_mfma<false,SP_IN><<<dim3(NTI, 8, 2*SP_IN), 256, 0, stream>>>(
-            inS, inG, inG, DPROJ, DM);
+
+        const unsigned short* wih_s = winh + (size_t)(2*i+0)*DPROJ*DM;
+        const unsigned short* wil_s = winl + (size_t)(2*i+0)*DPROJ*DM;
+        const unsigned short* wih_g = winh + (size_t)(2*i+1)*DPROJ*DM;
+        const unsigned short* wil_g = winl + (size_t)(2*i+1)*DPROJ*DM;
+        const unsigned short* woh_s = wouth + (size_t)(2*i+0)*DM*DIN;
+        const unsigned short* wol_s = woutl + (size_t)(2*i+0)*DM*DIN;
+        const unsigned short* woh_g = wouth + (size_t)(2*i+1)*DM*DIN;
+        const unsigned short* wol_g = woutl + (size_t)(2*i+1)*DM*DIN;
+
+        GemmJob inS{xsh, xsl, wih_s, wil_s, part_inS, RS};
+        GemmJob inG{xgh, xgl, wih_g, wil_g, part_inG, RG};
+        gemm_mfma<SP_IN><<<dim3(37, 8, 2*SP_IN), 256, 0, stream>>>(inS, inG, inG, DPROJ, DM);
 
         PrepJob pjS{part_inS, zsilu_s, xh_s, Bc_s, Cc_s, dtw_s, cw_s, cbv_s, dtb_s, RS, LS};
         PrepJob pjG{part_inG, zsilu_g, xh_g, Bc_g, Cc_g, dtw_g, cw_g, cbv_g, dtb_g, RG, LG};
@@ -793,49 +893,48 @@
             cbt_g, xh_g, dtw_g, al_g, Dw_g, y_g);
 
         gated_rmsnorm<<<dim3(RS+RG), 256, 0, stream>>>(
-            y_s, zsilu_s, nw_s, yn_s,  y_g, zsilu_g, nw_g, yn_g);
-
-        GemmJob outS{yn_s, Wout_s, part_outS, RS};
-        GemmJob outG{yn_g, Wout_g, part_outG, RG};
-        gemm_mfma<false,SP_OUT><<<dim3(DM/64, 8, 2*SP_OUT), 256, 0, stream>>>(
-            outS, outG, outG, DM, DIN);
-
-        RJob roS{part_outS, nullptr, nullptr, xs, RS};
-        RJob roG{part_outG, nullptr, nullptr, xg, RG};
+            y_s, zsilu_s, nw_s, ynh_s, ynl_s,  y_g, zsilu_g, nw_g, ynh_g, ynl_g);
+
+        GemmJob outS{ynh_s, ynl_s, woh_s, wol_s, part_outS, RS};
+        GemmJob outG{ynh_g, ynl_g, woh_g, wol_g, part_outG, RG};
+        gemm_mfma<SP_OUT><<<dim3(8, 8, 2*SP_OUT), 256, 0, stream>>>(outS, outG, outG, DM, DIN);
+
+        RJob roS{part_outS, nullptr, nullptr, xs, xsh, xsl, RS};
+        RJob roG{part_outG, nullptr, nullptr, xg, xgh, xgl, RG};
         reduce_k<SP_OUT><<<dim3(rblkS, 2), 256, 0, stream>>>(roS, roG, DM);
     }
 
     {
-        ln_rows<<<dim3(RS), 256, 0, stream>>>(xs, cas_ln_w, cas_ln_b, lnbuf, DM);
-        GemmJob jq{lnbuf, cas_in_w,            part_q, RS};
-        GemmJob jk{xg,    cas_in_w +  512*512, part_k, RG};
-        GemmJob jv{xg,    cas_in_w + 1024*512, part_v, RG};
-        gemm_mfma<true,SP_ATT><<<dim3(DM/64, 8, 3*SP_ATT), 256, 0, stream>>>(jq, jk, jv, DM, DM);
-        RJob rq{part_q, cas_in_b,      nullptr, qh, RS};
-        RJob rk{part_k, cas_in_b+512,  nullptr, kh, RG};
-        RJob rv{part_v, cas_in_b+1024, nullptr, vh, RG};
+        ln_rows<<<dim3(RS), 256, 0, stream>>>(xs, cas_ln_w, cas_ln_b, lnh, lnl, DM);
+        GemmJob jq{lnh, lnl, caih,            cail,            part_q, RS};
+        GemmJob jk{xgh, xgl, caih +  512*512, cail +  512*512, part_k, RG};
+        GemmJob jv{xgh, xgl, caih + 1024*512, cail + 1024*512, part_v, RG};
+        gemm_mfma<SP_ATT><<<dim3(8, 8, 3*SP_ATT), 256, 0, stream>>>(jq, jk, jv, DM, DM);
+        RJob rq{part_q, cas_in_b,      nullptr, qh, nullptr, nullptr, RS};
+        RJob rk{part_k, cas_in_b+512,  nullptr, kh, nullptr, nullptr, RG};
+        RJob rv{part_v, cas_in_b+1024, nullptr, vh, nullptr, nullptr, RG};
         reduce_k3<SP_ATT><<<dim3(rblkS, 3), 256, 0, stream>>>(rq, rk, rv, DM);
-        mha_attn2<LS,LG><<<dim3(8,BB), 256, 0, stream>>>(qh, kh, vh, attn_out);
-        GemmJob jo{attn_out, cas_out_w, part_outS, RS};
-        gemm_mfma<true,SP_ATT><<<dim3(DM/64, 8, SP_ATT), 256, 0, stream>>>(jo, jo, jo, DM, DM);
-        RJob ro{part_outS, cas_out_b, xs, xs, RS};
+        mha_attn2<LS,LG><<<dim3(8,BB), 256, 0, stream>>>(qh, kh, vh, aoh, aol);
+        GemmJob jo{aoh, aol, caoh, caol, part_outS, RS};
+        gemm_mfma<SP_ATT><<<dim3(8, 8, SP_ATT), 256, 0, stream>>>(jo, jo, jo, DM, DM);
+        RJob ro{part_outS, cas_out_b, xs, xs, xsh, xsl, RS};
         reduce_k<SP_ATT><<<dim3(rblkS, 1), 256, 0, stream>>>(ro, ro, DM);
     }
 
     {
-        ln_rows<<<dim3(RG), 256, 0, stream>>>(xg, cag_ln_w, cag_ln_b, lnbuf, DM);
-        GemmJob jq{lnbuf, cag_in_w,            part_q, RG};
-        GemmJob jk{xs,    cag_in_w +  512*512, part_k, RS};
-        GemmJob jv{xs,    cag_in_w + 1024*512, part_v, RS};
-        gemm_mfma<true,SP_ATT><<<dim3(DM/64, 8, 3*SP_ATT), 256, 0, stream>>>(jq, jk, jv, DM, DM);
-        RJob rq{part_q, cag_in_b,      nullptr, qh, RG};
-        RJob rk{part_k, cag_in_b+512,  nullptr, kh, RS};
-        RJob rv{part_v, cag_in_b+1024, nullptr, vh, RS};
+        ln_rows<<<dim3(RG), 256, 0, stream>>>(xg, cag_ln_w, cag_ln_b, lnh, lnl, DM);
+        GemmJob jq{lnh, lnl, cgih,            cgil,            part_q, RG};
+        GemmJob jk{xsh, xsl, cgih +  512*512, cgil +  512*512, part_k, RS};
+        GemmJob jv{xsh, xsl, cgih + 1024*512, cgil + 1024*512, part_v, RS};
+        gemm_mfma<SP_ATT><<<dim3(8, 8, 3*SP_ATT), 256, 0, stream>>>(jq, jk, jv, DM, DM);
+        RJob rq{part_q, cag_in_b,      nullptr, qh, nullptr, nullptr, RG};
+        RJob rk{part_k, cag_in_b+512,  nullptr, kh, nullptr, nullptr, RS};
+        RJob rv{part_v, cag_in_b+1024, nullptr, vh, nullptr, nullptr, RS};
         reduce_k3<SP_ATT><<<dim3(rblkS, 3), 256, 0, stream>>>(rq, rk, rv, DM);
-        mha_attn2<LG,LS><<<dim3(8,BB), 256, 0, stream>>>(qh, kh, vh, attn_out);
-        GemmJob jo{attn_out, cag_out_w, part_outS, RG};
-        gemm_mfma<true,SP_ATT><<<dim3(DM/64, 2, SP_ATT), 256, 0, stream>>>(jo, jo, jo, DM, DM);
-        RJob ro{part_outS, cag_out_b, xg, xg, RG};
+        mha_attn2<LG,LS><<<dim3(8,BB), 256, 0, stream>>>(qh, kh, vh, aoh, aol);
+        GemmJob jo{aoh, aol, cgoh, cgol, part_outS, RG};
+        gemm_mfma<SP_ATT><<<dim3(8, 2, SP_ATT), 256, 0, stream>>>(jo, jo, jo, DM, DM);
+        RJob ro{part_outS, cag_out_b, xg, xg, nullptr, nullptr, RG};
         reduce_k<SP_ATT><<<dim3((RG*DM+1023)/1024, 1), 256, 0, stream>>>(ro, ro, DM);
     }
 
```

Result: faster. 765.3 us (-8.8%).
